# Kernel tuning notes

Hardware: AMD Instinct MI355X
Metric: run time of the kernel (lower is better)

## Reference

```python
import jax, jax.numpy as jnp
import numpy as np
import math

B, P, C, PS = 128, 196, 3, 16      # batch, num_patchs, channels, patch_size
HID, HEADS, HD, FF = 768, 12, 64, 3072
RATE = PS // 4                      # highpass_rate = 4 -> rate = 4
EPS = 1e-5


def _local_highpass(x):
    # x: (B, P, HID) -> per-patch FFT highpass, matching LocalHighPass+HighPass.
    img = x.reshape(B, P, C, PS, PS)
    f = jnp.fft.fftshift(jnp.fft.fft2(img, norm='ortho'), axes=(-2, -1))
    mid = PS // 2
    f = f.at[..., mid - RATE:mid + RATE, mid - RATE:mid + RATE].set(0.0)
    out = jnp.fft.ifft2(jnp.fft.ifftshift(f, axes=(-2, -1)), norm='ortho').real
    return out.reshape(B, P, HID)


def _layernorm(x, g, b):
    m = x.mean(-1, keepdims=True)
    v = ((x - m) ** 2).mean(-1, keepdims=True)
    return (x - m) * jax.lax.rsqrt(v + EPS) * g + b


def setup_inputs() -> dict:
    key = jax.random.key(0)
    ks = jax.random.split(key, 16)
    s_h = 1.0 / math.sqrt(HID)
    s_f = 1.0 / math.sqrt(FF)
    inp = {
        'x': jax.random.normal(ks[0], (B, P, HID), jnp.float32),
        'q_w': jax.random.uniform(ks[1], (HID, HID), jnp.float32, -s_h, s_h),
        'q_b': jnp.zeros((HID,), jnp.float32),
        'k_w': jax.random.uniform(ks[2], (HID, HID), jnp.float32, -s_h, s_h),
        'k_b': jnp.zeros((HID,), jnp.float32),
        'v_w': jax.random.uniform(ks[3], (HID, HID), jnp.float32, -s_h, s_h),
        'v_b': jnp.zeros((HID,), jnp.float32),
        'w1': jax.random.uniform(ks[4], (FF, HID), jnp.float32, -s_h, s_h),
        'b1': jnp.zeros((FF,), jnp.float32),
        'w2': jax.random.uniform(ks[5], (HID, FF), jnp.float32, -s_f, s_f),
        'b2': jnp.zeros((HID,), jnp.float32),
        'ln0_g': jnp.ones((HID,), jnp.float32), 'ln0_b': jnp.zeros((HID,), jnp.float32),
        'ln1_g': jnp.ones((HID,), jnp.float32), 'ln1_b': jnp.zeros((HID,), jnp.float32),
        'ln2_g': jnp.ones((HID,), jnp.float32), 'ln2_b': jnp.zeros((HID,), jnp.float32),
    }
    return inp


def reference(x, q_w, q_b, k_w, k_b, v_w, v_b, w1, b1, w2, b2,
              ln0_g, ln0_b, ln1_g, ln1_b, ln2_g, ln2_b):
    hp = _local_highpass(x)                              # (B, P, HID)
    h = _layernorm(hp, ln0_g, ln0_b)
    # MSAttention (first_block=False, so no position embedding add)
    q = (h @ q_w.T + q_b).reshape(B, P, HEADS, HD)
    k = (h @ k_w.T + k_b).reshape(B, P, HEADS, HD)
    v = (h @ v_w.T + v_b).reshape(B, P, HEADS, HD)
    scores = jnp.einsum('bqhd,bkhd->bhqk', q, k) / math.sqrt(HD)
    probs = jax.nn.softmax(scores, axis=-1)
    ctx = jnp.einsum('bhqk,bkhd->bqhd', probs, v).reshape(B, P, HID)
    h2 = hp + _layernorm(ctx, ln1_g, ln1_b)
    mlp = jax.nn.relu(h2 @ w1.T + b1) @ w2.T + b2
    return h2 + _layernorm(mlp, ln2_g, ln2_b)
```

## Files before the change

kernel.cpp:

```cpp
#include <hip/hip_runtime.h>

#define NTOK   25088
#define HIDD   768
#define NHEAD  12
#define HDIM   64
#define FFD    3072
#define NPAT   196
#define QKVS   2304

typedef __attribute__((ext_vector_type(8))) short short8;
typedef __attribute__((ext_vector_type(8))) __bf16 bf16x8;
typedef __attribute__((ext_vector_type(4))) float f32x4;
typedef __attribute__((ext_vector_type(4))) float fl4;
typedef __attribute__((ext_vector_type(4))) unsigned short us4;
typedef __attribute__((ext_vector_type(8))) unsigned short us8;

#define AS1 __attribute__((address_space(1)))
#define AS3 __attribute__((address_space(3)))

__device__ __forceinline__ unsigned short f2bf(float f) {
  unsigned int u = __builtin_bit_cast(unsigned int, f);
  u += 0x7FFFu + ((u >> 16) & 1u);
  return (unsigned short)(u >> 16);
}
__device__ __forceinline__ float bf2f(unsigned short h) {
  unsigned int u = ((unsigned int)h) << 16;
  return __builtin_bit_cast(float, u);
}

template <typename A>
__device__ __forceinline__ auto mfma_sel(A a, A b, f32x4 c, int)
    -> decltype(__builtin_amdgcn_mfma_f32_16x16x32_bf16(a, b, c, 0, 0, 0)) {
  return __builtin_amdgcn_mfma_f32_16x16x32_bf16(a, b, c, 0, 0, 0);
}
template <typename A>
__device__ __forceinline__ auto mfma_sel(A a, A b, f32x4 c, long)
    -> decltype(__builtin_amdgcn_mfma_f32_16x16x32_bf16(
           __builtin_bit_cast(bf16x8, a), __builtin_bit_cast(bf16x8, b), c, 0, 0, 0)) {
  return __builtin_amdgcn_mfma_f32_16x16x32_bf16(
      __builtin_bit_cast(bf16x8, a), __builtin_bit_cast(bf16x8, b), c, 0, 0, 0);
}
__device__ __forceinline__ f32x4 MFMA16(short8 a, short8 b, f32x4 c) {
  return mfma_sel(a, b, c, 0);
}

__device__ __forceinline__ void gload16(const void* g, void* l) {
  __builtin_amdgcn_global_load_lds((const AS1 void*)g, (AS3 void*)l, 16, 0, 0);
}

__device__ __forceinline__ int swz_bid(int nwg) {
  int orig = (int)blockIdx.x;
  int xcd = orig & 7;
  int q = nwg >> 3, r = nwg & 7;
  int base = (xcd < r) ? xcd * (q + 1) : r * (q + 1) + (xcd - r) * q;
  return base + (orig >> 3);
}

__global__ __launch_bounds__(256) void build_M(unsigned short* __restrict__ Mb) {
  __shared__ float Cs[16], Ss[16];
  int t = threadIdx.x;
  if (t < 16) {
    float c = 0.f;
    for (int k = -4; k <= 3; ++k) c += cosf(0.39269908169872414f * (float)(k * t));
    Cs[t] = c;
    Ss[t] = -sinf(1.5707963267948966f * (float)t);
  }
  __syncthreads();
  int r = t >> 4, cc = t & 15;
  for (int j = 0; j < 256; ++j) {
    int dr = (r - (j >> 4)) & 15;
    int dc = (cc - (j & 15)) & 15;
    float val = ((t == j) ? 1.f : 0.f) - (Cs[dr] * Cs[dc] - Ss[dr] * Ss[dc]) * 0.00390625f;
    Mb[t * 256 + j] = f2bf(val);
  }
}

__global__ __launch_bounds__(256) void castk(const float* __restrict__ s,
                                             unsigned short* __restrict__ d, long n4) {
  for (long i = (long)blockIdx.x * 256 + threadIdx.x; i < n4; i += (long)gridDim.x * 256) {
    fl4 v = *(const fl4*)(s + i * 4);
    us4 o;
    o[0] = f2bf(v[0]); o[1] = f2bf(v[1]); o[2] = f2bf(v[2]); o[3] = f2bf(v[3]);
    *(us4*)(d + i * 4) = o;
  }
}

__global__ __launch_bounds__(256) void bias_cat(const float* __restrict__ qb,
                                                const float* __restrict__ kb,
                                                const float* __restrict__ vb,
                                                float* __restrict__ d) {
  for (int i = threadIdx.x; i < QKVS; i += 256)
    d[i] = (i < 768) ? qb[i] : (i < 1536) ? kb[i - 768] : vb[i - 1536];
}

template <int OUT_BF16, int BIAS, int RELU>
__global__ __launch_bounds__(512, 2) void gemm256(const unsigned short* __restrict__ A,
                                                  const unsigned short* __restrict__ Bm,
                                                  const float* __restrict__ bias,
                                                  void* __restrict__ Cp,
                                                  int Mdim, int Ndim, int Kdim) {
  __shared__ __align__(16) char lds[131072];
  const int nbn = Ndim >> 8;
  const int bid = swz_bid((int)gridDim.x);
  const int bm = bid / nbn, bn = bid % nbn;
  const int t = threadIdx.x;
  const int lane = t & 63, w = t >> 6;
  const int wm = w >> 2, wn = w & 3;
  const int lm = lane & 15, lg = lane >> 4;
  const int NT = Kdim >> 6, NITER = NT >> 1;

  const int tr = t >> 3;
  const int scol = ((t & 7) ^ (tr & 7)) * 8;
  const unsigned short* Asrc = A + (size_t)(bm * 256 + tr) * Kdim + scol;
  const unsigned short* Bsrc = Bm + (size_t)(bn * 256 + tr) * Kdim + scol;
  const size_t K64 = (size_t)64 * Kdim, K128 = (size_t)128 * Kdim, K192 = (size_t)192 * Kdim;

  auto SA = [&](int kt, int d) {
    char* dst = lds + d * 65536;
    const unsigned short* s = Asrc + kt * 64;
    gload16(s, dst + t * 16);
    gload16(s + K64, dst + 8192 + t * 16);
    gload16(s + K128, dst + 16384 + t * 16);
    gload16(s + K192, dst + 24576 + t * 16);
  };
  auto SB = [&](int kt, int d, int h) {
    char* dst = lds + d * 65536 + 32768 + h * 16384;
    const unsigned short* s = Bsrc + kt * 64 + (h ? K128 : 0);
    gload16(s, dst + t * 16);
    gload16(s + K64, dst + 8192 + t * 16);
  };

  const int sx = lm & 7;
  int slotb[2];
#pragma unroll
  for (int kk = 0; kk < 2; ++kk) slotb[kk] = (((kk << 2) | lg) ^ sx) << 4;
  const int aoff = wm * 16384 + lm * 128;
  const int boff = 32768 + (wn >> 1) * 16384 + ((wn & 1) * 64 + lm) * 128;

  f32x4 acc[8][4];
#pragma unroll
  for (int i = 0; i < 8; ++i)
#pragma unroll
    for (int j = 0; j < 4; ++j) acc[i][j] = (f32x4){0.f, 0.f, 0.f, 0.f};
  short8 bq[4][2];

  auto RDB = [&](const char* db) {
#pragma unroll
    for (int ni = 0; ni < 4; ++ni)
#pragma unroll
      for (int kk = 0; kk < 2; ++kk)
        bq[ni][kk] = *(const short8*)(db + boff + ni * 2048 + slotb[kk]);
  };
  auto MFMAQ = [&](const char* db, int q, int vmc) {
    short8 aq[2][2];
#pragma unroll
    for (int m2 = 0; m2 < 2; ++m2)
#pragma unroll
      for (int kk = 0; kk < 2; ++kk)
        aq[m2][kk] = *(const short8*)(db + aoff + q * 4096 + m2 * 2048 + slotb[kk]);
    __builtin_amdgcn_s_barrier();
    asm volatile("s_waitcnt lgkmcnt(0)" ::: "memory");
    __builtin_amdgcn_sched_barrier(0);
    __builtin_amdgcn_s_setprio(1);
#pragma unroll
    for (int kk = 0; kk < 2; ++kk)
#pragma unroll
      for (int m2 = 0; m2 < 2; ++m2)
#pragma unroll
        for (int ni = 0; ni < 4; ++ni)
          acc[q * 2 + m2][ni] = MFMA16(aq[m2][kk], bq[ni][kk], acc[q * 2 + m2][ni]);
    __builtin_amdgcn_s_setprio(0);
    if (vmc == 4) asm volatile("s_waitcnt vmcnt(4)" ::: "memory");
    else if (vmc == 0) asm volatile("s_waitcnt vmcnt(0)" ::: "memory");
    __builtin_amdgcn_s_barrier();
    __builtin_amdgcn_sched_barrier(0);
  };

  SA(0, 0); SB(0, 0, 0); SB(0, 0, 1); SB(1, 1, 0); SB(1, 1, 1);
  asm volatile("s_waitcnt vmcnt(4)" ::: "memory");
  __builtin_amdgcn_s_barrier();
  __builtin_amdgcn_sched_barrier(0);

  char* d0 = lds;
  char* d1 = lds + 65536;
  for (int j = 0; j < NITER; ++j) {
    const bool nl = (j + 1 < NITER);
    const int t2 = 2 * j + 2, t3 = 2 * j + 3;
    RDB(d0); SA(2 * j + 1, 1);   MFMAQ(d0, 0, -1);
    if (nl) SB(t2, 0, 0);        MFMAQ(d0, 1, -1);
    if (nl) SB(t2, 0, 1);        MFMAQ(d0, 2, -1);
                                 MFMAQ(d0, 3, nl ? 4 : 0);
    RDB(d1); if (nl) SA(t2, 0);  MFMAQ(d1, 0, -1);
    if (nl) SB(t3, 1, 0);        MFMAQ(d1, 1, -1);
    if (nl) SB(t3, 1, 1);        MFMAQ(d1, 2, -1);
                                 MFMAQ(d1, 3, nl ? 4 : -1);
  }

  const int row0 = bm * 256 + wm * 128 + lg * 4;
  const int col0 = bn * 256 + wn * 64 + lm;
#pragma unroll
  for (int mi = 0; mi < 8; ++mi) {
#pragma unroll
    for (int ni = 0; ni < 4; ++ni) {
      int col = col0 + ni * 16;
      float bia = BIAS ? bias[col] : 0.f;
#pragma unroll
      for (int rg = 0; rg < 4; ++rg) {
        int row = row0 + mi * 16 + rg;
        float vv = acc[mi][ni][rg] + bia;
        if (RELU) vv = vv > 0.f ? vv : 0.f;
        if (OUT_BF16)
          ((unsigned short*)Cp)[(size_t)row * Ndim + col] = f2bf(vv);
        else
          ((float*)Cp)[(size_t)row * Ndim + col] = vv;
      }
    }
  }
}

__global__ __launch_bounds__(256) void ln0_k(const unsigned short* __restrict__ x,
                                             const float* __restrict__ g,
                                             const float* __restrict__ bb,
                                             unsigned short* __restrict__ out) {
  int w = threadIdx.x >> 6, lane = threadIdx.x & 63;
  long row = (long)blockIdx.x * 4 + w;
  const unsigned short* xr = x + row * HIDD;
  float xv[12];
  float s1 = 0.f, s2 = 0.f;
#pragma unroll
  for (int c = 0; c < 3; ++c) {
    us4 u = *(const us4*)(xr + c * 256 + lane * 4);
#pragma unroll
    for (int j = 0; j < 4; ++j) {
      float f = bf2f(u[j]);
      xv[c * 4 + j] = f; s1 += f; s2 += f * f;
    }
  }
#pragma unroll
  for (int off = 32; off; off >>= 1) { s1 += __shfl_xor(s1, off); s2 += __shfl_xor(s2, off); }
  float m = s1 * (1.f / 768.f);
  float rs = rsqrtf(s2 * (1.f / 768.f) - m * m + 1e-5f);
#pragma unroll
  for (int c = 0; c < 3; ++c) {
    int cb = c * 256 + lane * 4;
    us4 o;
#pragma unroll
    for (int j = 0; j < 4; ++j) o[j] = f2bf((xv[c * 4 + j] - m) * rs * g[cb + j] + bb[cb + j]);
    *(us4*)(out + row * HIDD + cb) = o;
  }
}

__global__ __launch_bounds__(256) void ln1_k(const unsigned short* __restrict__ ctx,
                                             const unsigned short* __restrict__ hp,
                                             const float* __restrict__ g,
                                             const float* __restrict__ bb,
                                             float* __restrict__ h2f,
                                             unsigned short* __restrict__ h2b) {
  int w = threadIdx.x >> 6, lane = threadIdx.x & 63;
  long row = (long)blockIdx.x * 4 + w;
  const unsigned short* xr = ctx + row * HIDD;
  float xv[12];
  float s1 = 0.f, s2 = 0.f;
#pragma unroll
  for (int c = 0; c < 3; ++c) {
    us4 u = *(const us4*)(xr + c * 256 + lane * 4);
#pragma unroll
    for (int j = 0; j < 4; ++j) {
      float f = bf2f(u[j]);
      xv[c * 4 + j] = f; s1 += f; s2 += f * f;
    }
  }
#pragma unroll
  for (int off = 32; off; off >>= 1) { s1 += __shfl_xor(s1, off); s2 += __shfl_xor(s2, off); }
  float m = s1 * (1.f / 768.f);
  float rs = rsqrtf(s2 * (1.f / 768.f) - m * m + 1e-5f);
#pragma unroll
  for (int c = 0; c < 3; ++c) {
    int cb = c * 256 + lane * 4;
    us4 hv = *(const us4*)(hp + row * HIDD + cb);
    fl4 o;
    us4 ob;
#pragma unroll
    for (int j = 0; j < 4; ++j) {
      float y = bf2f(hv[j]) + (xv[c * 4 + j] - m) * rs * g[cb + j] + bb[cb + j];
      o[j] = y; ob[j] = f2bf(y);
    }
    *(fl4*)(h2f + row * HIDD + cb) = o;
    *(us4*)(h2b + row * HIDD + cb) = ob;
  }
}

__global__ __launch_bounds__(256) void ln2_k(float* __restrict__ mlp2_out,
                                             const float* __restrict__ h2f,
                                             const float* __restrict__ g,
                                             const float* __restrict__ bb) {
  int w = threadIdx.x >> 6, lane = threadIdx.x & 63;
  long row = (long)blockIdx.x * 4 + w;
  float* xr = mlp2_out + row * HIDD;
  fl4 v[3];
  float s1 = 0.f, s2 = 0.f;
#pragma unroll
  for (int c = 0; c < 3; ++c) {
    v[c] = *(const fl4*)(xr + c * 256 + lane * 4);
#pragma unroll
    for (int j = 0; j < 4; ++j) { s1 += v[c][j]; s2 += v[c][j] * v[c][j]; }
  }
#pragma unroll
  for (int off = 32; off; off >>= 1) { s1 += __shfl_xor(s1, off); s2 += __shfl_xor(s2, off); }
  float m = s1 * (1.f / 768.f);
  float rs = rsqrtf(s2 * (1.f / 768.f) - m * m + 1e-5f);
#pragma unroll
  for (int c = 0; c < 3; ++c) {
    int cb = c * 256 + lane * 4;
    fl4 hv = *(const fl4*)(h2f + row * HIDD + cb);
    fl4 o;
#pragma unroll
    for (int j = 0; j < 4; ++j) o[j] = hv[j] + (v[c][j] - m) * rs * g[cb + j] + bb[cb + j];
    *(fl4*)(xr + cb) = o;
  }
}

__global__ __launch_bounds__(256, 2) void attn_k(const unsigned short* __restrict__ qkv,
                                                 unsigned short* __restrict__ ctx) {
  __shared__ __align__(16) unsigned short Ks[NPAT * 64];
  __shared__ __align__(16) unsigned short VT[64 * 232];
  __shared__ __align__(16) unsigned short PL[4][16 * 40];
  const int b = blockIdx.x / NHEAD, h = blockIdx.x % NHEAD;
  const int t = threadIdx.x, lane = t & 63, w = t >> 6;
  const size_t base = ((size_t)b * NPAT) * QKVS + h * HDIM;

  for (int idx = t; idx < NPAT * 8; idx += 256) {
    int row = idx >> 3, s = idx & 7;
    us8 kv = *(const us8*)&qkv[base + 768 + (size_t)row * QKVS + s * 8];
    *(us8*)((char*)Ks + row * 128 + ((s ^ (row & 7)) << 4)) = kv;
  }
  for (int idx = t; idx < 98 * 64; idx += 256) {
    int pp = idx >> 6, d = idx & 63;
    unsigned int val = (unsigned int)qkv[base + 1536 + (size_t)(2 * pp) * QKVS + d]
                     | ((unsigned int)qkv[base + 1536 + (size_t)(2 * pp + 1) * QKVS + d] << 16);
    *(unsigned int*)&VT[d * 232 + 2 * pp] = val;
  }
  for (int idx = t; idx < 64 * 18; idx += 256) {
    int d = idx / 18, c = idx % 18;
    *(unsigned int*)&VT[d * 232 + 196 + 2 * c] = 0;
  }
  __syncthreads();

  unsigned short* plw = (unsigned short*)PL[w];
  const int lm = lane & 15, lg = lane >> 4, lk = lg * 8;

  for (int qt = w; qt < 13; qt += 4) {
    const int q0 = qt * 16;
    int qrow = q0 + lm; if (qrow > NPAT - 1) qrow = NPAT - 1;
    short8 af0 = *(const short8*)&qkv[base + (size_t)qrow * QKVS + lk];
    short8 af1 = *(const short8*)&qkv[base + (size_t)qrow * QKVS + 32 + lk];

    f32x4 sc[13];
#pragma unroll
    for (int kt = 0; kt < 13; ++kt) {
      int krow = kt * 16 + lm; if (krow > NPAT - 1) krow = NPAT - 1;
      const char* krp = (const char*)Ks + krow * 128;
      short8 b0 = *(const short8*)(krp + (((lg ^ (krow & 7)) & 7) << 4));
      short8 b1 = *(const short8*)(krp + ((((lg + 4) ^ (krow & 7)) & 7) << 4));
      f32x4 z = (f32x4){0.f, 0.f, 0.f, 0.f};
      z = MFMA16(af0, b0, z);
      sc[kt] = MFMA16(af1, b1, z);
    }
#pragma unroll
    for (int kt = 0; kt < 13; ++kt) {
      int col = kt * 16 + lm;
#pragma unroll
      for (int rg = 0; rg < 4; ++rg) {
        float s = sc[kt][rg] * 0.125f;
        sc[kt][rg] = (col < NPAT) ? s : -1e30f;
      }
    }
    float inv[4];
#pragma unroll
    for (int rg = 0; rg < 4; ++rg) {
      float m = -1e30f;
#pragma unroll
      for (int kt = 0; kt < 13; ++kt) m = fmaxf(m, sc[kt][rg]);
      m = fmaxf(m, __shfl_xor(m, 1)); m = fmaxf(m, __shfl_xor(m, 2));
      m = fmaxf(m, __shfl_xor(m, 4)); m = fmaxf(m, __shfl_xor(m, 8));
      float s = 0.f;
#pragma unroll
      for (int kt = 0; kt < 13; ++kt) { float e = __expf(sc[kt][rg] - m); sc[kt][rg] = e; s += e; }
      s += __shfl_xor(s, 1); s += __shfl_xor(s, 2); s += __shfl_xor(s, 4); s += __shfl_xor(s, 8);
      inv[rg] = 1.f / s;
    }

    f32x4 oacc[4];
#pragma unroll
    for (int ni = 0; ni < 4; ++ni) oacc[ni] = (f32x4){0.f, 0.f, 0.f, 0.f};
#pragma unroll
    for (int kc = 0; kc < 7; ++kc) {
#pragma unroll
      for (int sub = 0; sub < 2; ++sub) {
        const int kt = 2 * kc + sub;
#pragma unroll
        for (int rg = 0; rg < 4; ++rg) {
          unsigned short pv_ = 0;
          if (kt < 13) pv_ = f2bf(sc[kt][rg] * inv[rg]);
          plw[(lg * 4 + rg) * 40 + sub * 16 + lm] = pv_;
        }
      }
      asm volatile("s_waitcnt lgkmcnt(0)" ::: "memory");
      __builtin_amdgcn_sched_barrier(0);
      short8 pa = *(const short8*)&plw[lm * 40 + lk];
#pragma unroll
      for (int ni = 0; ni < 4; ++ni) {
        short8 bv = *(const short8*)&VT[(ni * 16 + lm) * 232 + kc * 32 + lk];
        oacc[ni] = MFMA16(pa, bv, oacc[ni]);
      }
    }
#pragma unroll
    for (int rg = 0; rg < 4; ++rg) {
      int r = q0 + lg * 4 + rg;
      if (r < NPAT) {
#pragma unroll
        for (int ni = 0; ni < 4; ++ni)
          ctx[((size_t)b * NPAT + r) * HIDD + h * HDIM + ni * 16 + lm] = f2bf(oacc[ni][rg]);
      }
    }
  }
}

extern "C" void kernel_launch(void* const* d_in, const int* in_sizes, int n_in,
                              void* d_out, int out_size, void* d_ws, size_t ws_size,
                              hipStream_t stream) {
  const float* x    = (const float*)d_in[0];
  const float* q_w  = (const float*)d_in[1];
  const float* q_b  = (const float*)d_in[2];
  const float* k_w  = (const float*)d_in[3];
  const float* k_b  = (const float*)d_in[4];
  const float* v_w  = (const float*)d_in[5];
  const float* v_b  = (const float*)d_in[6];
  const float* w1   = (const float*)d_in[7];
  const float* b1   = (const float*)d_in[8];
  const float* w2   = (const float*)d_in[9];
  const float* b2   = (const float*)d_in[10];
  const float* ln0g = (const float*)d_in[11];
  const float* ln0b = (const float*)d_in[12];
  const float* ln1g = (const float*)d_in[13];
  const float* ln1b = (const float*)d_in[14];
  const float* ln2g = (const float*)d_in[15];
  const float* ln2b = (const float*)d_in[16];

  char* ws = (char*)d_ws;
  size_t o = 0;
  auto alloc = [&](size_t bytes) { size_t r = o; o += (bytes + 255) & ~(size_t)255; return r; };

  const size_t RSZ = (size_t)NTOK * HIDD * 2;
  unsigned short* Mb    = (unsigned short*)(ws + alloc(256 * 256 * 2));
  unsigned short* wqkvb = (unsigned short*)(ws + alloc((size_t)QKVS * HIDD * 2));
  unsigned short* w1b   = (unsigned short*)(ws + alloc((size_t)FFD * HIDD * 2));
  unsigned short* w2b   = (unsigned short*)(ws + alloc((size_t)HIDD * FFD * 2));
  float*          qkvbias = (float*)(ws + alloc(QKVS * 4));
  char* r0 = ws + alloc(RSZ);
  char* r1 = ws + alloc(RSZ);
  char* r2 = ws + alloc(RSZ);
  char* r3 = ws + alloc(RSZ);
  char* r4 = ws + alloc(RSZ);
  char* r5 = ws + alloc(RSZ);
  (void)r5; (void)n_in; (void)in_sizes; (void)ws_size;

  unsigned short* xb  = (unsigned short*)r0;
  unsigned short* hpb = (unsigned short*)r1;
  unsigned short* hb  = (unsigned short*)r2;
  unsigned short* qkv = (unsigned short*)r3;
  unsigned short* cxb = (unsigned short*)r0;
  float*          h2f = (float*)r4;
  unsigned short* h2b = (unsigned short*)r2;
  unsigned short* m1b = (unsigned short*)r0;
  float*          m2f = (float*)d_out;

  build_M<<<1, 256, 0, stream>>>(Mb);
  bias_cat<<<1, 256, 0, stream>>>(q_b, k_b, v_b, qkvbias);

  auto cgrid = [](long n4) { long g = (n4 + 255) / 256; return (int)(g > 2048 ? 2048 : g); };
  long nx4 = (long)NTOK * HIDD / 4;
  castk<<<cgrid(nx4), 256, 0, stream>>>(x, xb, nx4);
  long nw4 = (long)HIDD * HIDD / 4;
  castk<<<cgrid(nw4), 256, 0, stream>>>(q_w, wqkvb, nw4);
  castk<<<cgrid(nw4), 256, 0, stream>>>(k_w, wqkvb + (size_t)768 * HIDD, nw4);
  castk<<<cgrid(nw4), 256, 0, stream>>>(v_w, wqkvb + (size_t)1536 * HIDD, nw4);
  long nf4 = (long)FFD * HIDD / 4;
  castk<<<cgrid(nf4), 256, 0, stream>>>(w1, w1b, nf4);
  castk<<<cgrid(nf4), 256, 0, stream>>>(w2, w2b, nf4);

  gemm256<1, 0, 0><<<294, 512, 0, stream>>>(xb, Mb, nullptr, hpb, 75264, 256, 256);
  ln0_k<<<NTOK / 4, 256, 0, stream>>>(hpb, ln0g, ln0b, hb);

  gemm256<1, 1, 0><<<98 * 9, 512, 0, stream>>>(hb, wqkvb, qkvbias, qkv, NTOK, QKVS, HIDD);

  attn_k<<<128 * NHEAD, 256, 0, stream>>>(qkv, cxb);

  ln1_k<<<NTOK / 4, 256, 0, stream>>>(cxb, hpb, ln1g, ln1b, h2f, h2b);

  for (int ch = 0; ch < 2; ++ch) {
    const unsigned short* h2c = h2b + (size_t)ch * 12544 * HIDD;
    float* m2c = m2f + (size_t)ch * 12544 * HIDD;
    gemm256<1, 1, 1><<<49 * 12, 512, 0, stream>>>(h2c, w1b, b1, m1b, 12544, FFD, HIDD);
    gemm256<0, 1, 0><<<49 * 3, 512, 0, stream>>>(m1b, w2b, b2, m2c, 12544, HIDD, FFD);
  }

  ln2_k<<<NTOK / 4, 256, 0, stream>>>(m2f, h2f, ln2g, ln2b);
  (void)out_size;
}
```

Baseline: 645.3 us.

## Double-buffer B fragments in GEMM, drop fp32 residual copy, unchunk MLP

```diff
diff --git a/kernel.cpp b/kernel.cpp
--- a/kernel.cpp
+++ b/kernel.cpp
@@ -115,6 +115,9 @@
   const unsigned short* Bsrc = Bm + (size_t)(bn * 256 + tr) * Kdim + scol;
   const size_t K64 = (size_t)64 * Kdim, K128 = (size_t)128 * Kdim, K192 = (size_t)192 * Kdim;
 
+  char* const d0 = lds;
+  char* const d1 = lds + 65536;
+
   auto SA = [&](int kt, int d) {
     char* dst = lds + d * 65536;
     const unsigned short* s = Asrc + kt * 64;
@@ -142,16 +145,16 @@
   for (int i = 0; i < 8; ++i)
 #pragma unroll
     for (int j = 0; j < 4; ++j) acc[i][j] = (f32x4){0.f, 0.f, 0.f, 0.f};
-  short8 bq[4][2];
-
-  auto RDB = [&](const char* db) {
+  short8 bqA[4][2], bqB[4][2];
+
+  auto RDB = [&](const char* db, short8 (&bq)[4][2]) {
 #pragma unroll
     for (int ni = 0; ni < 4; ++ni)
 #pragma unroll
       for (int kk = 0; kk < 2; ++kk)
         bq[ni][kk] = *(const short8*)(db + boff + ni * 2048 + slotb[kk]);
   };
-  auto MFMAQ = [&](const char* db, int q, int vmc) {
+  auto PH = [&](const char* db, int q, short8 (&bq)[4][2], int vmc) {
     short8 aq[2][2];
 #pragma unroll
     for (int m2 = 0; m2 < 2; ++m2)
@@ -170,7 +173,8 @@
         for (int ni = 0; ni < 4; ++ni)
           acc[q * 2 + m2][ni] = MFMA16(aq[m2][kk], bq[ni][kk], acc[q * 2 + m2][ni]);
     __builtin_amdgcn_s_setprio(0);
-    if (vmc == 4) asm volatile("s_waitcnt vmcnt(4)" ::: "memory");
+    if (vmc == 8)      asm volatile("s_waitcnt vmcnt(8)" ::: "memory");
+    else if (vmc == 4) asm volatile("s_waitcnt vmcnt(4)" ::: "memory");
     else if (vmc == 0) asm volatile("s_waitcnt vmcnt(0)" ::: "memory");
     __builtin_amdgcn_s_barrier();
     __builtin_amdgcn_sched_barrier(0);
@@ -180,20 +184,19 @@
   asm volatile("s_waitcnt vmcnt(4)" ::: "memory");
   __builtin_amdgcn_s_barrier();
   __builtin_amdgcn_sched_barrier(0);
-
-  char* d0 = lds;
-  char* d1 = lds + 65536;
+  RDB(d0, bqA);
+
   for (int j = 0; j < NITER; ++j) {
     const bool nl = (j + 1 < NITER);
     const int t2 = 2 * j + 2, t3 = 2 * j + 3;
-    RDB(d0); SA(2 * j + 1, 1);   MFMAQ(d0, 0, -1);
-    if (nl) SB(t2, 0, 0);        MFMAQ(d0, 1, -1);
-    if (nl) SB(t2, 0, 1);        MFMAQ(d0, 2, -1);
-                                 MFMAQ(d0, 3, nl ? 4 : 0);
-    RDB(d1); if (nl) SA(t2, 0);  MFMAQ(d1, 0, -1);
-    if (nl) SB(t3, 1, 0);        MFMAQ(d1, 1, -1);
-    if (nl) SB(t3, 1, 1);        MFMAQ(d1, 2, -1);
-                                 MFMAQ(d1, 3, nl ? 4 : -1);
+    SA(2 * j + 1, 1);       PH(d0, 0, bqA, -1);
+    if (nl) SB(t2, 0, 0);   PH(d0, 1, bqA, -1);
+    if (nl) SB(t2, 0, 1);   PH(d0, 2, bqA, nl ? 8 : 4);
+    RDB(d1, bqB);           PH(d0, 3, bqA, nl ? 4 : 0);
+    if (nl) SA(t2, 0);      PH(d1, 0, bqB, -1);
+    if (nl) SB(t3, 1, 0);   PH(d1, 1, bqB, -1);
+    if (nl) SB(t3, 1, 1);   PH(d1, 2, bqB, nl ? 8 : -1);
+    if (nl) RDB(d0, bqA);   PH(d1, 3, bqB, nl ? 4 : -1);
   }
 
   const int row0 = bm * 256 + wm * 128 + lg * 4;
@@ -254,7 +257,6 @@
                                              const unsigned short* __restrict__ hp,
                                              const float* __restrict__ g,
                                              const float* __restrict__ bb,
-                                             float* __restrict__ h2f,
                                              unsigned short* __restrict__ h2b) {
   int w = threadIdx.x >> 6, lane = threadIdx.x & 63;
   long row = (long)blockIdx.x * 4 + w;
@@ -278,20 +280,16 @@
   for (int c = 0; c < 3; ++c) {
     int cb = c * 256 + lane * 4;
     us4 hv = *(const us4*)(hp + row * HIDD + cb);
-    fl4 o;
     us4 ob;
 #pragma unroll
-    for (int j = 0; j < 4; ++j) {
-      float y = bf2f(hv[j]) + (xv[c * 4 + j] - m) * rs * g[cb + j] + bb[cb + j];
-      o[j] = y; ob[j] = f2bf(y);
-    }
-    *(fl4*)(h2f + row * HIDD + cb) = o;
+    for (int j = 0; j < 4; ++j)
+      ob[j] = f2bf(bf2f(hv[j]) + (xv[c * 4 + j] - m) * rs * g[cb + j] + bb[cb + j]);
     *(us4*)(h2b + row * HIDD + cb) = ob;
   }
 }
 
 __global__ __launch_bounds__(256) void ln2_k(float* __restrict__ mlp2_out,
-                                             const float* __restrict__ h2f,
+                                             const unsigned short* __restrict__ h2b,
                                              const float* __restrict__ g,
                                              const float* __restrict__ bb) {
   int w = threadIdx.x >> 6, lane = threadIdx.x & 63;
@@ -312,10 +310,11 @@
 #pragma unroll
   for (int c = 0; c < 3; ++c) {
     int cb = c * 256 + lane * 4;
-    fl4 hv = *(const fl4*)(h2f + row * HIDD + cb);
+    us4 hv = *(const us4*)(h2b + row * HIDD + cb);
     fl4 o;
 #pragma unroll
-    for (int j = 0; j < 4; ++j) o[j] = hv[j] + (v[c][j] - m) * rs * g[cb + j] + bb[cb + j];
+    for (int j = 0; j < 4; ++j)
+      o[j] = bf2f(hv[j]) + (v[c][j] - m) * rs * g[cb + j] + bb[cb + j];
     *(fl4*)(xr + cb) = o;
   }
 }
@@ -457,22 +456,21 @@
   unsigned short* w1b   = (unsigned short*)(ws + alloc((size_t)FFD * HIDD * 2));
   unsigned short* w2b   = (unsigned short*)(ws + alloc((size_t)HIDD * FFD * 2));
   float*          qkvbias = (float*)(ws + alloc(QKVS * 4));
-  char* r0 = ws + alloc(RSZ);
-  char* r1 = ws + alloc(RSZ);
-  char* r2 = ws + alloc(RSZ);
-  char* r3 = ws + alloc(RSZ);
-  char* r4 = ws + alloc(RSZ);
-  char* r5 = ws + alloc(RSZ);
-  (void)r5; (void)n_in; (void)in_sizes; (void)ws_size;
-
-  unsigned short* xb  = (unsigned short*)r0;
-  unsigned short* hpb = (unsigned short*)r1;
-  unsigned short* hb  = (unsigned short*)r2;
-  unsigned short* qkv = (unsigned short*)r3;
-  unsigned short* cxb = (unsigned short*)r0;
-  float*          h2f = (float*)r4;
-  unsigned short* h2b = (unsigned short*)r2;
-  unsigned short* m1b = (unsigned short*)r0;
+  char* rA  = ws + alloc(RSZ);
+  char* rB  = ws + alloc(RSZ);
+  char* rC0 = ws + alloc(RSZ);
+  char* rC1 = ws + alloc(RSZ);
+  char* rC2 = ws + alloc(RSZ);
+  char* rC3 = ws + alloc(RSZ);
+  (void)rC2; (void)rC3; (void)n_in; (void)in_sizes; (void)ws_size;
+
+  unsigned short* xb  = (unsigned short*)rC0;
+  unsigned short* hpb = (unsigned short*)rA;
+  unsigned short* hb  = (unsigned short*)rB;
+  unsigned short* qkv = (unsigned short*)rC1;
+  unsigned short* cxb = (unsigned short*)rC0;
+  unsigned short* h2b = (unsigned short*)rB;
+  unsigned short* m1b = (unsigned short*)rC0;
   float*          m2f = (float*)d_out;
 
   build_M<<<1, 256, 0, stream>>>(Mb);
@@ -496,15 +494,11 @@
 
   attn_k<<<128 * NHEAD, 256, 0, stream>>>(qkv, cxb);
 
-  ln1_k<<<NTOK / 4, 256, 0, stream>>>(cxb, hpb, ln1g, ln1b, h2f, h2b);
-
-  for (int ch = 0; ch < 2; ++ch) {
-    const unsigned short* h2c = h2b + (size_t)ch * 12544 * HIDD;
-    float* m2c = m2f + (size_t)ch * 12544 * HIDD;
-    gemm256<1, 1, 1><<<49 * 12, 512, 0, stream>>>(h2c, w1b, b1, m1b, 12544, FFD, HIDD);
-    gemm256<0, 1, 0><<<49 * 3, 512, 0, stream>>>(m1b, w2b, b2, m2c, 12544, HIDD, FFD);
-  }
-
-  ln2_k<<<NTOK / 4, 256, 0, stream>>>(m2f, h2f, ln2g, ln2b);
+  ln1_k<<<NTOK / 4, 256, 0, stream>>>(cxb, hpb, ln1g, ln1b, h2b);
+
+  gemm256<1, 1, 1><<<98 * 12, 512, 0, stream>>>(h2b, w1b, b1, m1b, NTOK, FFD, HIDD);
+  gemm256<0, 1, 0><<<98 * 3, 512, 0, stream>>>(m1b, w2b, b2, m2f, NTOK, HIDD, FFD);
+
+  ln2_k<<<NTOK / 4, 256, 0, stream>>>(m2f, h2b, ln2g, ln2b);
   (void)out_size;
 }
```

Result: faster. 628.3 us (-2.6%).
